# Kernel tuning notes

Hardware: AMD Instinct MI355X
Metric: run time of the kernel (lower is better)

Reference implementation:

```python
import jax, jax.numpy as jnp
import numpy as np

B, T, L, H = 8, 32, 512, 768  # batch docs, decode steps, encoder length, BART-base hidden


def setup_inputs() -> dict:
    key = jax.random.key(0)
    ks = jax.random.split(key, 7)
    sc = 1.0 / np.sqrt(H).astype(np.float32)
    return {
        "encoder_hn": jax.random.normal(ks[0], (B, L, H), jnp.float32),
        "dec": jax.random.normal(ks[1], (B, T, H), jnp.float32),   # decoder_rnn outputs per step
        "W1": jax.random.normal(ks[2], (H, H), jnp.float32) * sc,  # nnW1 (no bias)
        "W2": jax.random.normal(ks[3], (H, H), jnp.float32) * sc,  # nnW2 (no bias)
        "v": jax.random.normal(ks[4], (H,), jnp.float32) * sc,     # nnV (no bias)
        "starts": jax.random.randint(ks[5], (B, T), 0, 128, jnp.int32),  # ragged slice start per step
        "lens": jax.random.randint(ks[6], (B,), 300, L + 1, jnp.int32),  # curL per document
    }


def reference(encoder_hn, dec, W1, W2, v, starts, lens):
    # pointerLayer batched over (b, t):
    #   WE = nnW1(en)          -> [B, L, H]
    #   WD = nnW2(di expanded) -> [B, T, H]
    #   scores = selu( nnV( selu(WE + WD) ) )  over positions [start, len)
    WE = jnp.einsum('blh,kh->blk', encoder_hn, W1)                 # [B, L, H]
    WD = jnp.einsum('bth,kh->btk', dec, W2)                        # [B, T, H]
    act = jax.nn.selu(WE[:, None, :, :] + WD[:, :, None, :])      # [B, T, L, H]
    scores = jax.nn.selu(jnp.einsum('btlh,h->btl', act, v))       # [B, T, L]
    # ragged slice curencoder_hn[start:curL] expressed as a mask
    pos = jnp.arange(L, dtype=jnp.int32)
    mask = (pos[None, None, :] >= starts[:, :, None]) & \
           (pos[None, None, :] < lens[:, None, None])              # [B, T, L]
    NEG = jnp.asarray(-1e30, scores.dtype)
    logp = jax.nn.log_softmax(jnp.where(mask, scores, NEG), axis=-1)
    return jnp.where(mask, logp, jnp.zeros((), logp.dtype))       # masked log-probs [B, T, L]
```

## Files before the change

kernel.cpp:

```cpp
#include <hip/hip_runtime.h>
#include <math.h>

constexpr int Bn = 8, Tn = 32, Ln = 512, Hn = 768;

typedef __attribute__((ext_vector_type(8))) short bf16x8;
typedef __attribute__((ext_vector_type(4))) float f32x4;

__device__ __forceinline__ short f2bf(float x) {
    unsigned u = __float_as_uint(x);
    u += 0x7FFFu + ((u >> 16) & 1u);
    return (short)(u >> 16);
}
__device__ __forceinline__ float bf2f(unsigned short s) {
    return __uint_as_float(((unsigned)s) << 16);
}

constexpr float kScale = 1.0507009873554804934193349852946f;
constexpr float kAS    = 1.7580993408473768f;

__device__ __forceinline__ float selu(float x) {
    return x > 0.f ? kScale * x : fmaf(kAS, __expf(x), -kAS);
}

__global__ __launch_bounds__(256) void cvt_bf16_multi(
    const float* __restrict__ s0, short* __restrict__ d0, int c0,
    const float* __restrict__ s1, short* __restrict__ d1, int c1,
    const float* __restrict__ s2, short* __restrict__ d2, int c2,
    const float* __restrict__ s3, short* __restrict__ d3, int c3)
{
    const int i = blockIdx.x * 256 + threadIdx.x;
    if (i >= c3) return;
    const float* s; short* d; int off;
    if (i < c0)      { s = s0; d = d0; off = i; }
    else if (i < c1) { s = s1; d = d1; off = i - c0; }
    else if (i < c2) { s = s2; d = d2; off = i - c1; }
    else             { s = s3; d = d3; off = i - c2; }
    const float4 f = ((const float4*)s)[off];
    short4 r;
    r.x = f2bf(f.x); r.y = f2bf(f.y); r.z = f2bf(f.z); r.w = f2bf(f.w);
    ((short4*)d)[off] = r;
}

__global__ __launch_bounds__(256) void gemm2_bf16_nt(
    const short* __restrict__ A1, const short* __restrict__ B1,
    unsigned short* __restrict__ C1, int M1,
    const short* __restrict__ A2, const short* __restrict__ B2,
    unsigned short* __restrict__ C2,
    int N, int K)
{
    constexpr int BM = 128, BN = 128, BK = 32;
    __shared__ __align__(16) short As[2][BM * BK];
    __shared__ __align__(16) short Bs[2][BN * BK];

    const int nblk1 = M1 / BM;
    const int bx = blockIdx.x;
    const short* A; const short* Bm; unsigned short* C; int bm;
    if (bx < nblk1) { A = A1; Bm = B1; C = C1; bm = bx * BM; }
    else            { A = A2; Bm = B2; C = C2; bm = (bx - nblk1) * BM; }
    const int bn = blockIdx.y * BN;

    const int tid  = threadIdx.x;
    const int lane = tid & 63;
    const int wv   = tid >> 6;
    const int quad = lane >> 4;
    const int l16  = lane & 15;
    const int wm   = (wv & 1) * 64;
    const int wn   = (wv >> 1) * 64;

    const int sr = lane >> 2;
    const int kq = (lane & 3) << 3;
    const int ra = wv * 16 + sr;

    f32x4 acc[4][4] = {};

    auto stage = [&](int buf, int k0) {
        __builtin_amdgcn_global_load_lds(
            (const __attribute__((address_space(1))) unsigned int*)(A + (size_t)(bm + ra) * K + k0 + kq),
            (__attribute__((address_space(3))) unsigned int*)(&As[buf][ra * BK + kq]), 16, 0, 0);
        __builtin_amdgcn_global_load_lds(
            (const __attribute__((address_space(1))) unsigned int*)(A + (size_t)(bm + 64 + ra) * K + k0 + kq),
            (__attribute__((address_space(3))) unsigned int*)(&As[buf][(64 + ra) * BK + kq]), 16, 0, 0);
        __builtin_amdgcn_global_load_lds(
            (const __attribute__((address_space(1))) unsigned int*)(Bm + (size_t)(bn + ra) * K + k0 + kq),
            (__attribute__((address_space(3))) unsigned int*)(&Bs[buf][ra * BK + kq]), 16, 0, 0);
        __builtin_amdgcn_global_load_lds(
            (const __attribute__((address_space(1))) unsigned int*)(Bm + (size_t)(bn + 64 + ra) * K + k0 + kq),
            (__attribute__((address_space(3))) unsigned int*)(&Bs[buf][(64 + ra) * BK + kq]), 16, 0, 0);
    };

    stage(0, 0);
    __syncthreads();

    for (int k0 = 0; k0 < K; k0 += BK) {
        const int cur = (k0 / BK) & 1;
        const int nxt = cur ^ 1;
        if (k0 + BK < K) stage(nxt, k0 + BK);

        bf16x8 af[4], bfr[4];
#pragma unroll
        for (int i = 0; i < 4; ++i)
            af[i] = *(const bf16x8*)&As[cur][(wm + i * 16 + l16) * BK + quad * 8];
#pragma unroll
        for (int j = 0; j < 4; ++j)
            bfr[j] = *(const bf16x8*)&Bs[cur][(wn + j * 16 + l16) * BK + quad * 8];
#pragma unroll
        for (int i = 0; i < 4; ++i)
#pragma unroll
            for (int j = 0; j < 4; ++j)
                acc[i][j] = __builtin_amdgcn_mfma_f32_16x16x32_bf16(af[i], bfr[j], acc[i][j], 0, 0, 0);
        __syncthreads();
    }

#pragma unroll
    for (int i = 0; i < 4; ++i)
#pragma unroll
        for (int j = 0; j < 4; ++j)
#pragma unroll
            for (int rr = 0; rr < 4; ++rr) {
                const int row = bm + wm + i * 16 + quad * 4 + rr;
                const int col = bn + wn + j * 16 + l16;
                C[(size_t)row * N + col] = (unsigned short)f2bf(acc[i][j][rr]);
            }
}

__global__ __launch_bounds__(1024) void scores_softmax_fused(
    const unsigned short* __restrict__ WE,
    const unsigned short* __restrict__ WD,
    const float* __restrict__ v,
    const int* __restrict__ starts,
    const int* __restrict__ lens,
    float* __restrict__ out)
{
    const int bid = blockIdx.x;
    const int b = bid & 7;
    const int t = bid >> 3;
    const int bt = b * Tn + t;
    const int tid = threadIdx.x;
    const int lane = tid & 63;
    const int wv = tid >> 6;

    __shared__ float sc[Ln];
    __shared__ float red[16];

    const int start = starts[bt];
    const int len = lens[b];

    float wdr[12], vr[12];
#pragma unroll
    for (int j = 0; j < 3; ++j) {
        const int h = (lane << 2) + (j << 8);
        const ushort4 wdu = *(const ushort4*)(WD + (size_t)bt * Hn + h);
        const float4 vv = *(const float4*)(v + h);
        wdr[j * 4 + 0] = bf2f(wdu.x); wdr[j * 4 + 1] = bf2f(wdu.y);
        wdr[j * 4 + 2] = bf2f(wdu.z); wdr[j * 4 + 3] = bf2f(wdu.w);
        vr[j * 4 + 0] = vv.x; vr[j * 4 + 1] = vv.y;
        vr[j * 4 + 2] = vv.z; vr[j * 4 + 3] = vv.w;
    }

    const unsigned short* WEb = WE + (size_t)b * Ln * Hn;

    for (int k = 0; k < 8; ++k) {
        const int g = wv + (k << 4);
        const int lg = g << 2;
        if (lg + 3 < start || lg >= len) continue;

        ushort4 weu[4][3];
#pragma unroll
        for (int rr = 0; rr < 4; ++rr) {
            const unsigned short* row = WEb + (size_t)(lg + rr) * Hn;
#pragma unroll
            for (int j = 0; j < 3; ++j)
                weu[rr][j] = *(const ushort4*)(row + (lane << 2) + (j << 8));
        }
        float s[4] = {0.f, 0.f, 0.f, 0.f};
#pragma unroll
        for (int j = 0; j < 3; ++j) {
#pragma unroll
            for (int rr = 0; rr < 4; ++rr) {
                float x;
                x = bf2f(weu[rr][j].x) + wdr[j * 4 + 0]; s[rr] = fmaf(selu(x), vr[j * 4 + 0], s[rr]);
                x = bf2f(weu[rr][j].y) + wdr[j * 4 + 1]; s[rr] = fmaf(selu(x), vr[j * 4 + 1], s[rr]);
                x = bf2f(weu[rr][j].z) + wdr[j * 4 + 2]; s[rr] = fmaf(selu(x), vr[j * 4 + 2], s[rr]);
                x = bf2f(weu[rr][j].w) + wdr[j * 4 + 3]; s[rr] = fmaf(selu(x), vr[j * 4 + 3], s[rr]);
            }
        }
#pragma unroll
        for (int off = 32; off > 0; off >>= 1) {
#pragma unroll
            for (int rr = 0; rr < 4; ++rr)
                s[rr] += __shfl_xor(s[rr], off, 64);
        }
        if (lane == 0) {
#pragma unroll
            for (int rr = 0; rr < 4; ++rr)
                sc[lg + rr] = selu(s[rr]);
        }
    }
    __syncthreads();

    const int l = tid;
    const bool active = (l < Ln);
    const bool msk = active && (l >= start) && (l < len);
    const float val = msk ? sc[l] : -1e30f;

    float mx = val;
#pragma unroll
    for (int off = 32; off > 0; off >>= 1)
        mx = fmaxf(mx, __shfl_xor(mx, off, 64));
    if (lane == 0 && wv < 8) red[wv] = mx;
    __syncthreads();
    mx = red[0];
#pragma unroll
    for (int i = 1; i < 8; ++i) mx = fmaxf(mx, red[i]);

    float sm = msk ? __expf(val - mx) : 0.f;
#pragma unroll
    for (int off = 32; off > 0; off >>= 1)
        sm += __shfl_xor(sm, off, 64);
    if (lane == 0 && wv < 8) red[8 + wv] = sm;
    __syncthreads();
    float tot = red[8];
#pragma unroll
    for (int i = 1; i < 8; ++i) tot += red[8 + i];

    if (active) {
        const float logZ = mx + __logf(tot);
        out[(size_t)bt * Ln + l] = msk ? (val - logZ) : 0.f;
    }
}

extern "C" void kernel_launch(void* const* d_in, const int* in_sizes, int n_in,
                              void* d_out, int out_size, void* d_ws, size_t ws_size,
                              hipStream_t stream) {
    const float* enc    = (const float*)d_in[0];
    const float* dec    = (const float*)d_in[1];
    const float* W1     = (const float*)d_in[2];
    const float* W2     = (const float*)d_in[3];
    const float* v      = (const float*)d_in[4];
    const int*   starts = (const int*)d_in[5];
    const int*   lens   = (const int*)d_in[6];
    float* out = (float*)d_out;

    constexpr int n_enc = Bn * Ln * Hn;
    constexpr int n_dec = Bn * Tn * Hn;
    constexpr int n_w   = Hn * Hn;

    const size_t need = (size_t)(n_enc + n_dec + 2 * n_w) * 2
                      + (size_t)(n_enc + n_dec) * 2;
    if (ws_size < need) return;

    short* enc16 = (short*)d_ws;
    short* dec16 = enc16 + n_enc;
    short* w1_16 = dec16 + n_dec;
    short* w2_16 = w1_16 + n_w;
    unsigned short* WE16 = (unsigned short*)(w2_16 + n_w);
    unsigned short* WD16 = WE16 + n_enc;

    constexpr int c0 = n_enc / 4;
    constexpr int c1 = c0 + n_dec / 4;
    constexpr int c2 = c1 + n_w / 4;
    constexpr int c3 = c2 + n_w / 4;
    cvt_bf16_multi<<<dim3((c3 + 255) / 256), dim3(256), 0, stream>>>(
        enc, enc16, c0, dec, dec16, c1, W1, w1_16, c2, W2, w2_16, c3);

    gemm2_bf16_nt<<<dim3((Bn * Ln) / 128 + (Bn * Tn) / 128, Hn / 128),
                    dim3(256), 0, stream>>>(
        enc16, w1_16, WE16, Bn * Ln,
        dec16, w2_16, WD16, Hn, Hn);

    scores_softmax_fused<<<dim3(Bn * Tn), dim3(1024), 0, stream>>>(
        WE16, WD16, v, starts, lens, out);
}
```

Measured before the change: 125.5 us.

## Fuse fp32-to-bf16 conversion into GEMM staging and drop separate convert kernel

```diff
diff --git a/kernel.cpp b/kernel.cpp
--- a/kernel.cpp
+++ b/kernel.cpp
@@ -22,39 +22,27 @@
     return x > 0.f ? kScale * x : fmaf(kAS, __expf(x), -kAS);
 }
 
-__global__ __launch_bounds__(256) void cvt_bf16_multi(
-    const float* __restrict__ s0, short* __restrict__ d0, int c0,
-    const float* __restrict__ s1, short* __restrict__ d1, int c1,
-    const float* __restrict__ s2, short* __restrict__ d2, int c2,
-    const float* __restrict__ s3, short* __restrict__ d3, int c3)
-{
-    const int i = blockIdx.x * 256 + threadIdx.x;
-    if (i >= c3) return;
-    const float* s; short* d; int off;
-    if (i < c0)      { s = s0; d = d0; off = i; }
-    else if (i < c1) { s = s1; d = d1; off = i - c0; }
-    else if (i < c2) { s = s2; d = d2; off = i - c1; }
-    else             { s = s3; d = d3; off = i - c2; }
-    const float4 f = ((const float4*)s)[off];
-    short4 r;
-    r.x = f2bf(f.x); r.y = f2bf(f.y); r.z = f2bf(f.z); r.w = f2bf(f.w);
-    ((short4*)d)[off] = r;
-}
-
-__global__ __launch_bounds__(256) void gemm2_bf16_nt(
-    const short* __restrict__ A1, const short* __restrict__ B1,
+__device__ __forceinline__ bf16x8 pack8(float4 a, float4 b) {
+    bf16x8 r;
+    r[0] = f2bf(a.x); r[1] = f2bf(a.y); r[2] = f2bf(a.z); r[3] = f2bf(a.w);
+    r[4] = f2bf(b.x); r[5] = f2bf(b.y); r[6] = f2bf(b.z); r[7] = f2bf(b.w);
+    return r;
+}
+
+__global__ __launch_bounds__(256) void gemm2_f32_nt(
+    const float* __restrict__ A1, const float* __restrict__ B1,
     unsigned short* __restrict__ C1, int M1,
-    const short* __restrict__ A2, const short* __restrict__ B2,
+    const float* __restrict__ A2, const float* __restrict__ B2,
     unsigned short* __restrict__ C2,
     int N, int K)
 {
     constexpr int BM = 128, BN = 128, BK = 32;
-    __shared__ __align__(16) short As[2][BM * BK];
-    __shared__ __align__(16) short Bs[2][BN * BK];
+    __shared__ __align__(16) short As[BM * BK];
+    __shared__ __align__(16) short Bs[BN * BK];
 
     const int nblk1 = M1 / BM;
     const int bx = blockIdx.x;
-    const short* A; const short* Bm; unsigned short* C; int bm;
+    const float* A; const float* Bm; unsigned short* C; int bm;
     if (bx < nblk1) { A = A1; Bm = B1; C = C1; bm = bx * BM; }
     else            { A = A2; Bm = B2; C = C2; bm = (bx - nblk1) * BM; }
     const int bn = blockIdx.y * BN;
@@ -67,48 +55,61 @@
     const int wm   = (wv & 1) * 64;
     const int wn   = (wv >> 1) * 64;
 
-    const int sr = lane >> 2;
-    const int kq = (lane & 3) << 3;
-    const int ra = wv * 16 + sr;
+    int srow[2], skk[2];
+#pragma unroll
+    for (int p = 0; p < 2; ++p) {
+        const int unit = tid + (p << 8);
+        srow[p] = unit >> 2;
+        skk[p]  = (unit & 3) << 3;
+    }
 
     f32x4 acc[4][4] = {};
 
-    auto stage = [&](int buf, int k0) {
-        __builtin_amdgcn_global_load_lds(
-            (const __attribute__((address_space(1))) unsigned int*)(A + (size_t)(bm + ra) * K + k0 + kq),
-            (__attribute__((address_space(3))) unsigned int*)(&As[buf][ra * BK + kq]), 16, 0, 0);
-        __builtin_amdgcn_global_load_lds(
-            (const __attribute__((address_space(1))) unsigned int*)(A + (size_t)(bm + 64 + ra) * K + k0 + kq),
-            (__attribute__((address_space(3))) unsigned int*)(&As[buf][(64 + ra) * BK + kq]), 16, 0, 0);
-        __builtin_amdgcn_global_load_lds(
-            (const __attribute__((address_space(1))) unsigned int*)(Bm + (size_t)(bn + ra) * K + k0 + kq),
-            (__attribute__((address_space(3))) unsigned int*)(&Bs[buf][ra * BK + kq]), 16, 0, 0);
-        __builtin_amdgcn_global_load_lds(
-            (const __attribute__((address_space(1))) unsigned int*)(Bm + (size_t)(bn + 64 + ra) * K + k0 + kq),
-            (__attribute__((address_space(3))) unsigned int*)(&Bs[buf][(64 + ra) * BK + kq]), 16, 0, 0);
+    float4 cra[2][2], crb[2][2], nra[2][2], nrb[2][2];
+
+    auto gload = [&](float4 ra[2][2], float4 rb[2][2], int k0) {
+#pragma unroll
+        for (int p = 0; p < 2; ++p) {
+            const float* pa = A  + (size_t)(bm + srow[p]) * K + k0 + skk[p];
+            ra[p][0] = *(const float4*)pa;
+            ra[p][1] = *(const float4*)(pa + 4);
+            const float* pb = Bm + (size_t)(bn + srow[p]) * K + k0 + skk[p];
+            rb[p][0] = *(const float4*)pb;
+            rb[p][1] = *(const float4*)(pb + 4);
+        }
     };
 
-    stage(0, 0);
-    __syncthreads();
+    gload(cra, crb, 0);
 
     for (int k0 = 0; k0 < K; k0 += BK) {
-        const int cur = (k0 / BK) & 1;
-        const int nxt = cur ^ 1;
-        if (k0 + BK < K) stage(nxt, k0 + BK);
+        if (k0 + BK < K) gload(nra, nrb, k0 + BK);
+        if (k0 > 0) __syncthreads();
+#pragma unroll
+        for (int p = 0; p < 2; ++p) {
+            const int off = (tid + (p << 8)) << 3;
+            *(bf16x8*)&As[off] = pack8(cra[p][0], cra[p][1]);
+            *(bf16x8*)&Bs[off] = pack8(crb[p][0], crb[p][1]);
+        }
+        __syncthreads();
 
         bf16x8 af[4], bfr[4];
 #pragma unroll
         for (int i = 0; i < 4; ++i)
-            af[i] = *(const bf16x8*)&As[cur][(wm + i * 16 + l16) * BK + quad * 8];
+            af[i] = *(const bf16x8*)&As[(wm + i * 16 + l16) * BK + quad * 8];
 #pragma unroll
         for (int j = 0; j < 4; ++j)
-            bfr[j] = *(const bf16x8*)&Bs[cur][(wn + j * 16 + l16) * BK + quad * 8];
+            bfr[j] = *(const bf16x8*)&Bs[(wn + j * 16 + l16) * BK + quad * 8];
 #pragma unroll
         for (int i = 0; i < 4; ++i)
 #pragma unroll
             for (int j = 0; j < 4; ++j)
                 acc[i][j] = __builtin_amdgcn_mfma_f32_16x16x32_bf16(af[i], bfr[j], acc[i][j], 0, 0, 0);
-        __syncthreads();
+
+#pragma unroll
+        for (int p = 0; p < 2; ++p) {
+            cra[p][0] = nra[p][0]; cra[p][1] = nra[p][1];
+            crb[p][0] = nrb[p][0]; crb[p][1] = nrb[p][1];
+        }
     }
 
 #pragma unroll
@@ -243,30 +244,17 @@
 
     constexpr int n_enc = Bn * Ln * Hn;
     constexpr int n_dec = Bn * Tn * Hn;
-    constexpr int n_w   = Hn * Hn;
-
-    const size_t need = (size_t)(n_enc + n_dec + 2 * n_w) * 2
-                      + (size_t)(n_enc + n_dec) * 2;
+
+    const size_t need = (size_t)(n_enc + n_dec) * 2;
     if (ws_size < need) return;
 
-    short* enc16 = (short*)d_ws;
-    short* dec16 = enc16 + n_enc;
-    short* w1_16 = dec16 + n_dec;
-    short* w2_16 = w1_16 + n_w;
-    unsigned short* WE16 = (unsigned short*)(w2_16 + n_w);
+    unsigned short* WE16 = (unsigned short*)d_ws;
     unsigned short* WD16 = WE16 + n_enc;
 
-    constexpr int c0 = n_enc / 4;
-    constexpr int c1 = c0 + n_dec / 4;
-    constexpr int c2 = c1 + n_w / 4;
-    constexpr int c3 = c2 + n_w / 4;
-    cvt_bf16_multi<<<dim3((c3 + 255) / 256), dim3(256), 0, stream>>>(
-        enc, enc16, c0, dec, dec16, c1, W1, w1_16, c2, W2, w2_16, c3);
-
-    gemm2_bf16_nt<<<dim3((Bn * Ln) / 128 + (Bn * Tn) / 128, Hn / 128),
-                    dim3(256), 0, stream>>>(
-        enc16, w1_16, WE16, Bn * Ln,
-        dec16, w2_16, WD16, Hn, Hn);
+    gemm2_f32_nt<<<dim3((Bn * Ln) / 128 + (Bn * Tn) / 128, Hn / 128),
+                   dim3(256), 0, stream>>>(
+        enc, W1, WE16, Bn * Ln,
+        dec, W2, WD16, Hn, Hn);
 
     scores_softmax_fused<<<dim3(Bn * Tn), dim3(1024), 0, stream>>>(
         WE16, WD16, v, starts, lens, out);
```

Result: faster. 122.0 us (-2.8%).
